# Kernel optimization log

Measured on AMD Instinct MI355X. Metric: run time of the kernel, lower is better.

The kernel has to match this reference:

```python
import jax, jax.numpy as jnp
import numpy as np

N, X_DIM, Z_DIM, H = 4096, 256, 128, 512
NUM_ACTIONS = 4
TEMPERATURE = 0.1


def _init_linear(key, fan_in, fan_out):
    kw, kb = jax.random.split(key)
    bound = 1.0 / np.sqrt(fan_in)
    W = jax.random.uniform(kw, (fan_in, fan_out), minval=-bound, maxval=bound, dtype=jnp.float32)
    b = jax.random.uniform(kb, (fan_out,), minval=-bound, maxval=bound, dtype=jnp.float32)
    return W, b


def setup_inputs() -> dict:
    key = jax.random.key(0)
    ks = jax.random.split(key, 9)
    s = jax.random.normal(ks[0], (N, X_DIM), dtype=jnp.float32)
    sp = jax.random.normal(ks[1], (N, X_DIM), dtype=jnp.float32)
    a = jax.random.randint(ks[2], (N,), 0, NUM_ACTIONS)
    a1h = jax.nn.one_hot(a, NUM_ACTIONS, dtype=jnp.float32)
    # phi: x_dim -> 512 -> 512 -> z_dim
    pW0, pb0 = _init_linear(ks[3], X_DIM, H)
    pW1, pb1 = _init_linear(ks[4], H, H)
    pW2, pb2 = _init_linear(ks[5], H, Z_DIM)
    # g: x_dim + 4 -> 512 -> 512 -> z_dim
    gW0, gb0 = _init_linear(ks[6], X_DIM + NUM_ACTIONS, H)
    gW1, gb1 = _init_linear(ks[7], H, H)
    gW2, gb2 = _init_linear(ks[8], H, Z_DIM)
    return {"s": s, "sp": sp, "a1h": a1h,
            "pW0": pW0, "pb0": pb0, "pW1": pW1, "pb1": pb1, "pW2": pW2, "pb2": pb2,
            "gW0": gW0, "gb0": gb0, "gW1": gW1, "gb1": gb1, "gW2": gW2, "gb2": gb2}


def _mlp(x, W0, b0, W1, b1, W2, b2):
    h = jax.nn.relu(x @ W0 + b0)
    h = jax.nn.relu(h @ W1 + b1)
    return h @ W2 + b2


def reference(s, sp, a1h, pW0, pb0, pW1, pb1, pW2, pb2, gW0, gb0, gW1, gb1, gW2, gb2):
    z = _mlp(s, pW0, pb0, pW1, pb1, pW2, pb2)                      # [N, D]
    zpos = _mlp(jnp.concatenate([sp, a1h], axis=-1), gW0, gb0, gW1, gb1, gW2, gb2)  # [N, D]
    # -||z_i - zpos_j||^2 / T via the GEMM trick (avoids the [N,N,D] diff tensor)
    sq_z = jnp.sum(z * z, axis=-1, keepdims=True)                  # [N, 1]
    sq_p = jnp.sum(zpos * zpos, axis=-1)                            # [N]
    logits = -(sq_z + sq_p[None, :] - 2.0 * z @ zpos.T) / TEMPERATURE  # [N, N]
    # cross-entropy with targets = arange(N): diagonal is the positive
    log_probs = jax.nn.log_softmax(logits, axis=-1)
    loss = -jnp.mean(jnp.diagonal(log_probs))
    return loss
```

## Files before the change

### kernel.cpp

```cpp
#include <hip/hip_runtime.h>
#include <math.h>

#define NR 4096
#define HD 512
#define NJR 32
#define INV_T 10.0f

typedef __attribute__((ext_vector_type(8))) short bf16x8;
typedef __attribute__((ext_vector_type(4))) short short4v;
typedef __attribute__((ext_vector_type(4))) float f32x4;

typedef const unsigned int __attribute__((address_space(1)))* gas_t;
typedef unsigned int __attribute__((address_space(3)))* las_t;

__device__ __forceinline__ unsigned short f2bf(float f) {
  union { float f; unsigned u; } v; v.f = f;
  unsigned r = v.u + 0x7fff + ((v.u >> 16) & 1);
  return (unsigned short)(r >> 16);
}
__device__ __forceinline__ float bf2f(unsigned short b) {
  union { unsigned u; float f; } v; v.u = ((unsigned)b) << 16;
  return v.f;
}


__global__ __launch_bounds__(256) void prep(
    const float* __restrict__ s, const float* __restrict__ sp,
    const float* __restrict__ a1h,
    unsigned short* __restrict__ Sb, unsigned short* __restrict__ SPb,
    int* __restrict__ aidx, float* __restrict__ sqp,
    const float* __restrict__ pW0, unsigned short* __restrict__ pW0t,
    const float* __restrict__ pW1, unsigned short* __restrict__ pW1t,
    const float* __restrict__ pW2, unsigned short* __restrict__ pW2t,
    const float* __restrict__ gW0, unsigned short* __restrict__ gW0t,
    const float* __restrict__ gW1, unsigned short* __restrict__ gW1t,
    const float* __restrict__ gW2, unsigned short* __restrict__ gW2t,
    float* __restrict__ out) {
  int b = blockIdx.x, tid = threadIdx.x;
  if (b < 16) {
    int r = b * 256 + tid;
    int a = 0;
#pragma unroll
    for (int j = 0; j < 4; ++j) if (a1h[(size_t)r * 4 + j] > 0.5f) a = j;
    aidx[r] = a;
    sqp[r] = 0.f;
    if (b == 0 && tid == 0) out[0] = 0.f;
    return;
  }
  const int idx8 = tid & 127;
  const int h = idx8 & 1, p = idx8 >> 1, hi = p >> 4, l15 = p & 15;
  if (b < 2064) {
    const float* src = (b < 1040) ? s : sp;
    unsigned short* dst = (b < 1040) ? Sb : SPb;
    int lb = (b < 1040) ? b - 16 : b - 1040;
    int s0 = lb * 2 + (tid >> 7);
    int rf = s0 >> 3, ks = s0 & 7;
    int row = rf * 16 + l15, c0 = ks * 32 + hi * 4 + h * 16;
    float4 v = *(const float4*)&src[(size_t)row * 256 + c0];
    short4v o = { (short)f2bf(v.x), (short)f2bf(v.y), (short)f2bf(v.z), (short)f2bf(v.w) };
    *(short4v*)((char*)dst + (size_t)s0 * 1024 + idx8 * 8) = o;
    return;
  }
  int local = b - 2064;
  const float* W; unsigned short* Wt; int N, ksh;
  if (local < 128)      { W = pW0; Wt = pW0t; N = 512; ksh = 3; }
  else if (local < 384) { W = pW1; Wt = pW1t; N = 512; ksh = 4; local -= 128; }
  else if (local < 448) { W = pW2; Wt = pW2t; N = 128; ksh = 4; local -= 384; }
  else if (local < 576) { W = gW0; Wt = gW0t; N = 512; ksh = 3; local -= 448; }
  else if (local < 832) { W = gW1; Wt = gW1t; N = 512; ksh = 4; local -= 576; }
  else                  { W = gW2; Wt = gW2t; N = 128; ksh = 4; local -= 832; }
  int s0 = local * 2 + (tid >> 7);
  int rf = s0 >> ksh, ks = s0 & ((1 << ksh) - 1);
  int n = rf * 16 + l15, k0 = ks * 32 + hi * 4 + h * 16;
  short4v o = { (short)f2bf(W[(size_t)(k0 + 0) * N + n]),
                (short)f2bf(W[(size_t)(k0 + 1) * N + n]),
                (short)f2bf(W[(size_t)(k0 + 2) * N + n]),
                (short)f2bf(W[(size_t)(k0 + 3) * N + n]) };
  *(short4v*)((char*)Wt + (size_t)s0 * 1024 + idx8 * 8) = o;
}

template <int BM, int BN, int K, bool RELU, bool GB, bool SQ>
__global__ __launch_bounds__(256) void gemm_db(
    const unsigned short* __restrict__ A0, const unsigned short* __restrict__ A1,
    const unsigned short* __restrict__ W0, const unsigned short* __restrict__ W1,
    const float* __restrict__ b0, const float* __restrict__ b1,
    unsigned short* __restrict__ C0, unsigned short* __restrict__ C1,
    float* __restrict__ sqp, int N,
    const int* __restrict__ aidx, const float* __restrict__ gW0f) {
  constexpr int KS = K >> 5;
  constexpr int NSTEP = K >> 6;
  constexpr int ABY = BM * 128;
  constexpr int BBY = BN * 128;
  constexpr int RFW = BM >> 5;
  constexpr int FNW = BN >> 5;
  constexpr int V = RFW + FNW;
  __shared__ char lds[2 * (ABY + BBY)];
  char* As = lds;
  char* Bs = lds + 2 * ABY;

  const int tid = threadIdx.x, lane = tid & 63, w = tid >> 6;
  const int wm = w >> 1, wn = w & 1;
  const int z = blockIdx.z;
  const char* Ab = (const char*)(z ? A1 : A0);
  const char* Wb = (const char*)(z ? W1 : W0);
  const float* bias = z ? b1 : b0;
  char* Cb = (char*)(z ? C1 : C0);
  const int bm = blockIdx.x * BM, bn = blockIdx.y * BN;
  const int lane16 = lane * 16;

  auto stage = [&](int buf, int st) {
#pragma unroll
    for (int u = 0; u < RFW; ++u) {
      const int sl = w * RFW + u;
      const char* src = Ab + ((size_t)((bm >> 4) + (sl >> 1)) * KS + st * 2 + (sl & 1)) * 1024 + lane16;
      __builtin_amdgcn_global_load_lds((gas_t)src, (las_t)(As + buf * ABY + sl * 1024), 16, 0, 0);
    }
#pragma unroll
    for (int u = 0; u < FNW; ++u) {
      const int sl = w * FNW + u;
      const char* src = Wb + ((size_t)((bn >> 4) + (sl >> 1)) * KS + st * 2 + (sl & 1)) * 1024 + lane16;
      __builtin_amdgcn_global_load_lds((gas_t)src, (las_t)(Bs + buf * BBY + sl * 1024), 16, 0, 0);
    }
  };

  f32x4 acc[RFW][FNW] = {};
  stage(0, 0);
#pragma unroll
  for (int st = 0; st < NSTEP; ++st) {
    const int buf = st & 1;
    if (st + 1 < NSTEP) {
      stage(buf ^ 1, st + 1);
      if constexpr (V == 4) asm volatile("s_waitcnt vmcnt(4)" ::: "memory");
      else                  asm volatile("s_waitcnt vmcnt(3)" ::: "memory");
    } else {
      asm volatile("s_waitcnt vmcnt(0)" ::: "memory");
    }
    __builtin_amdgcn_s_barrier();
#pragma unroll
    for (int kss = 0; kss < 2; ++kss) {
      bf16x8 af[RFW], bfv[FNW];
#pragma unroll
      for (int i = 0; i < RFW; ++i)
        af[i] = *(const bf16x8*)(As + buf * ABY + ((wm * RFW + i) * 2 + kss) * 1024 + lane16);
#pragma unroll
      for (int j = 0; j < FNW; ++j)
        bfv[j] = *(const bf16x8*)(Bs + buf * BBY + ((wn * FNW + j) * 2 + kss) * 1024 + lane16);
#pragma unroll
      for (int i = 0; i < RFW; ++i)
#pragma unroll
        for (int j = 0; j < FNW; ++j)
          acc[i][j] = __builtin_amdgcn_mfma_f32_16x16x32_bf16(bfv[j], af[i], acc[i][j], 0, 0, 0);
    }
    __builtin_amdgcn_s_barrier();
  }

  const int l15 = lane & 15, hi = lane >> 4;
  const int NS = N >> 5;
  const int row0 = bm + wm * (RFW * 16);
  const int col0 = bn + wn * (FNW * 16);
  int ar[RFW];
#pragma unroll
  for (int i = 0; i < RFW; ++i) ar[i] = 0;
  if (GB && z == 1) {
#pragma unroll
    for (int i = 0; i < RFW; ++i) ar[i] = aidx[row0 + i * 16 + l15];
  }
  if constexpr (FNW == 2) {
    float4 bi0 = *(const float4*)&bias[col0 + hi * 4];
    float4 bi1 = *(const float4*)&bias[col0 + 16 + hi * 4];
#pragma unroll
    for (int i = 0; i < RFW; ++i) {
      const int rfC = (row0 >> 4) + i;
      float v[8] = { acc[i][0][0] + bi0.x, acc[i][0][1] + bi0.y,
                     acc[i][0][2] + bi0.z, acc[i][0][3] + bi0.w,
                     acc[i][1][0] + bi1.x, acc[i][1][1] + bi1.y,
                     acc[i][1][2] + bi1.z, acc[i][1][3] + bi1.w };
      if (GB && z == 1) {
        float4 g0 = *(const float4*)&gW0f[(size_t)(256 + ar[i]) * N + col0 + hi * 4];
        float4 g1 = *(const float4*)&gW0f[(size_t)(256 + ar[i]) * N + col0 + 16 + hi * 4];
        v[0] += g0.x; v[1] += g0.y; v[2] += g0.z; v[3] += g0.w;
        v[4] += g1.x; v[5] += g1.y; v[6] += g1.z; v[7] += g1.w;
      }
      bf16x8 r;
#pragma unroll
      for (int t = 0; t < 8; ++t) {
        float vv = RELU ? fmaxf(v[t], 0.f) : v[t];
        r[t] = (short)f2bf(vv);
      }
      *(bf16x8*)(Cb + (size_t)(rfC * NS + (col0 >> 5)) * 1024 + lane16) = r;
    }
  } else {
    float4 bi0 = *(const float4*)&bias[col0 + hi * 4];
    float sq[RFW];
#pragma unroll
    for (int i = 0; i < RFW; ++i) sq[i] = 0.f;
#pragma unroll
    for (int i = 0; i < RFW; ++i) {
      const int rfC = (row0 >> 4) + i;
      float v[4] = { acc[i][0][0] + bi0.x, acc[i][0][1] + bi0.y,
                     acc[i][0][2] + bi0.z, acc[i][0][3] + bi0.w };
      short4v r;
#pragma unroll
      for (int t = 0; t < 4; ++t) {
        float vv = RELU ? fmaxf(v[t], 0.f) : v[t];
        unsigned short cv = f2bf(vv);
        r[t] = (short)cv;
        if (SQ) { float vb = bf2f(cv); sq[i] += vb * vb; }
      }
      *(short4v*)(Cb + (size_t)(rfC * NS + (bn >> 5)) * 1024 + lane16 + wn * 8) = r;
    }
    if (SQ && z == 1) {
#pragma unroll
      for (int i = 0; i < RFW; ++i) {
        float t = sq[i];
        t += __shfl_xor(t, 16, 64);
        t += __shfl_xor(t, 32, 64);
        if (lane < 16) atomicAdd(&sqp[row0 + i * 16 + lane], t);
      }
    }
  }
}

__global__ __launch_bounds__(256) void logits_fm(
    const unsigned short* __restrict__ Zb, const unsigned short* __restrict__ Zpb,
    const float* __restrict__ sqp, float* __restrict__ wm_,
    float* __restrict__ wsum, float* __restrict__ wdiag) {
  const int tid = threadIdx.x, lane = tid & 63, w = tid >> 6;
  const int l15 = lane & 15, hi = lane >> 4;
  const int i0 = blockIdx.x * 128, jr = blockIdx.y;
  const int row32 = i0 + w * 32;
  const int jbase = jr * 128;
  const int lane16 = lane * 16;
  const char* Zc = (const char*)Zb;
  const char* Pc = (const char*)Zpb;

  bf16x8 afr[2][4];
#pragma unroll
  for (int rf = 0; rf < 2; ++rf)
#pragma unroll
    for (int ks = 0; ks < 4; ++ks)
      afr[rf][ks] = *(const bf16x8*)(Zc + (size_t)(((row32 >> 4) + rf) * 4 + ks) * 1024 + lane16);

  f32x4 acc[2][8] = {};
#pragma unroll
  for (int jf = 0; jf < 8; ++jf) {
    const size_t js = (size_t)((jbase >> 4) + jf) * 4;
#pragma unroll
    for (int ks = 0; ks < 4; ++ks) {
      bf16x8 bfv = *(const bf16x8*)(Pc + (js + ks) * 1024 + lane16);
      acc[0][jf] = __builtin_amdgcn_mfma_f32_16x16x32_bf16(bfv, afr[0][ks], acc[0][jf], 0, 0, 0);
      acc[1][jf] = __builtin_amdgcn_mfma_f32_16x16x32_bf16(bfv, afr[1][ks], acc[1][jf], 0, 0, 0);
    }
  }

#pragma unroll
  for (int rf = 0; rf < 2; ++rf) {
    const int grow = row32 + rf * 16 + l15;
    float mx = -INFINITY, dd = 0.f;
    bool hasd = false;
#pragma unroll
    for (int jf = 0; jf < 8; ++jf) {
      const int cb = jbase + jf * 16 + hi * 4;
      float4 q = *(const float4*)&sqp[cb];
      float sp[4] = { q.x, q.y, q.z, q.w };
#pragma unroll
      for (int e = 0; e < 4; ++e) {
        float lv = (2.f * acc[rf][jf][e] - sp[e]) * INV_T;
        acc[rf][jf][e] = lv;
        mx = fmaxf(mx, lv);
        if (cb + e == grow) { dd = lv; hasd = true; }
      }
    }
    mx = fmaxf(mx, __shfl_xor(mx, 16, 64));
    mx = fmaxf(mx, __shfl_xor(mx, 32, 64));
    float sum = 0.f;
#pragma unroll
    for (int jf = 0; jf < 8; ++jf)
#pragma unroll
      for (int e = 0; e < 4; ++e) sum += __expf(acc[rf][jf][e] - mx);
    sum += __shfl_xor(sum, 16, 64);
    sum += __shfl_xor(sum, 32, 64);
    if (hi == 0) {
      wm_[(size_t)jr * NR + grow] = mx;
      wsum[(size_t)jr * NR + grow] = sum;
    }
    if (hasd) wdiag[grow] = dd;
  }
}

__global__ __launch_bounds__(256) void finalize(const float* __restrict__ wm,
    const float* __restrict__ wsum, const float* __restrict__ wdiag,
    float* __restrict__ out) {
  int r = blockIdx.x * 256 + threadIdx.x;
  float mm = wm[r];
  float ss = wsum[r];
#pragma unroll
  for (int p = 1; p < NJR; ++p) {
    float mo = wm[(size_t)p * NR + r];
    float so = wsum[(size_t)p * NR + r];
    float mn = fmaxf(mm, mo);
    ss = ss * __expf(mm - mn) + so * __expf(mo - mn);
    mm = mn;
  }
  float loss_r = mm + logf(ss) - wdiag[r];
  float v = loss_r;
#pragma unroll
  for (int off = 32; off; off >>= 1) v += __shfl_xor(v, off, 64);
  __shared__ float partial[4];
  if ((threadIdx.x & 63) == 0) partial[threadIdx.x >> 6] = v;
  __syncthreads();
  if (threadIdx.x == 0)
    atomicAdd(out, (partial[0] + partial[1] + partial[2] + partial[3]) * (1.0f / (float)NR));
}

extern "C" void kernel_launch(void* const* d_in, const int* in_sizes, int n_in,
                              void* d_out, int out_size, void* d_ws, size_t ws_size,
                              hipStream_t stream) {
  const float* s   = (const float*)d_in[0];
  const float* sp  = (const float*)d_in[1];
  const float* a1h = (const float*)d_in[2];
  const float* pW0 = (const float*)d_in[3];
  const float* pb0 = (const float*)d_in[4];
  const float* pW1 = (const float*)d_in[5];
  const float* pb1 = (const float*)d_in[6];
  const float* pW2 = (const float*)d_in[7];
  const float* pb2 = (const float*)d_in[8];
  const float* gW0 = (const float*)d_in[9];
  const float* gb0 = (const float*)d_in[10];
  const float* gW1 = (const float*)d_in[11];
  const float* gb1 = (const float*)d_in[12];
  const float* gW2 = (const float*)d_in[13];
  const float* gb2 = (const float*)d_in[14];

  char* p = (char*)d_ws;
  unsigned short* Sb   = (unsigned short*)p; p += (size_t)NR * 256 * 2;
  unsigned short* SPb  = (unsigned short*)p; p += (size_t)NR * 256 * 2;
  unsigned short* H1   = (unsigned short*)p; p += (size_t)2 * NR * HD * 2;
  unsigned short* H2   = (unsigned short*)p; p += (size_t)2 * NR * HD * 2;
  unsigned short* Zall = (unsigned short*)p; p += (size_t)2 * NR * 128 * 2;
  unsigned short* pW0t = (unsigned short*)p; p += (size_t)256 * 512 * 2;
  unsigned short* pW1t = (unsigned short*)p; p += (size_t)512 * 512 * 2;
  unsigned short* pW2t = (unsigned short*)p; p += (size_t)512 * 128 * 2;
  unsigned short* gW0t = (unsigned short*)p; p += (size_t)256 * 512 * 2;
  unsigned short* gW1t = (unsigned short*)p; p += (size_t)512 * 512 * 2;
  unsigned short* gW2t = (unsigned short*)p; p += (size_t)512 * 128 * 2;
  float* sqp  = (float*)p; p += (size_t)NR * 4;
  float* wm   = (float*)p; p += (size_t)NJR * NR * 4;
  float* wsm  = (float*)p; p += (size_t)NJR * NR * 4;
  float* wdg  = (float*)p; p += (size_t)NR * 4;
  int*   aidx = (int*)p;  p += (size_t)NR * 4;

  unsigned short* H1g = H1 + (size_t)NR * HD;
  unsigned short* H2g = H2 + (size_t)NR * HD;
  unsigned short* Zb  = Zall;
  unsigned short* Zpb = Zall + (size_t)NR * 128;

  dim3 blk(256);
  prep<<<2960, blk, 0, stream>>>(s, sp, a1h, Sb, SPb, aidx, sqp,
                                 pW0, pW0t, pW1, pW1t, pW2, pW2t,
                                 gW0, gW0t, gW1, gW1t, gW2, gW2t,
                                 (float*)d_out);

  gemm_db<64, 64, 256, true, true, false><<<dim3(64, 8, 2), blk, 0, stream>>>(
      Sb, SPb, pW0t, gW0t, pb0, gb0, H1, H1g, nullptr, 512, aidx, gW0);
  gemm_db<64, 64, 512, true, false, false><<<dim3(64, 8, 2), blk, 0, stream>>>(
      H1, H1g, pW1t, gW1t, pb1, gb1, H2, H2g, nullptr, 512, nullptr, nullptr);
  gemm_db<64, 32, 512, false, false, true><<<dim3(64, 4, 2), blk, 0, stream>>>(
      H2, H2g, pW2t, gW2t, pb2, gb2, Zb, Zpb, sqp, 128, nullptr, nullptr);

  logits_fm<<<dim3(NR / 128, NJR), blk, 0, stream>>>(Zb, Zpb, sqp, wm, wsm, wdg);
  finalize<<<NR / 256, blk, 0, stream>>>(wm, wsm, wdg, (float*)d_out);
}
```

Baseline: 57.32 us.

## Fuse input conversion into layer-0 GEMM and finalize into logits kernel

The first layer now reads fp32 inputs and weights directly, converting to bf16 in registers and writing the tiled LDS layout itself. This removes the separate bf16 copies of s/sp and the W0 transposes, and folds the action-index decode into the epilogue. The squared-norm atomics become per-column-block partial sums, and the logits kernel now stages Zpos tiles in LDS. The last blocks of the logits kernel, chosen through an atomic counter with a spin-wait, run the final log-sum-exp reduction, which removes two launches. The trade-off is an uncoalesced scalar-scatter B write in layer 0 and a spin-wait that depends on all blocks being scheduled.

Result: slower. 69.25 us (+20.8%).

```diff
diff --git a/kernel.cpp b/kernel.cpp
--- a/kernel.cpp
+++ b/kernel.cpp
@@ -5,6 +5,7 @@
 #define HD 512
 #define NJR 32
 #define INV_T 10.0f
+#define DONE_FINAL 1024
 
 typedef __attribute__((ext_vector_type(8))) short bf16x8;
 typedef __attribute__((ext_vector_type(4))) short short4v;
@@ -24,80 +25,166 @@
 }
 
 
-__global__ __launch_bounds__(256) void prep(
+__global__ __launch_bounds__(256) void l0_fused(
     const float* __restrict__ s, const float* __restrict__ sp,
     const float* __restrict__ a1h,
-    unsigned short* __restrict__ Sb, unsigned short* __restrict__ SPb,
-    int* __restrict__ aidx, float* __restrict__ sqp,
-    const float* __restrict__ pW0, unsigned short* __restrict__ pW0t,
+    const float* __restrict__ pW0, const float* __restrict__ gW0,
+    const float* __restrict__ pb0, const float* __restrict__ gb0,
+    unsigned short* __restrict__ H1p, unsigned short* __restrict__ H1g,
     const float* __restrict__ pW1, unsigned short* __restrict__ pW1t,
     const float* __restrict__ pW2, unsigned short* __restrict__ pW2t,
-    const float* __restrict__ gW0, unsigned short* __restrict__ gW0t,
     const float* __restrict__ gW1, unsigned short* __restrict__ gW1t,
-    const float* __restrict__ gW2, unsigned short* __restrict__ gW2t,
-    float* __restrict__ out) {
-  int b = blockIdx.x, tid = threadIdx.x;
-  if (b < 16) {
-    int r = b * 256 + tid;
-    int a = 0;
-#pragma unroll
-    for (int j = 0; j < 4; ++j) if (a1h[(size_t)r * 4 + j] > 0.5f) a = j;
-    aidx[r] = a;
-    sqp[r] = 0.f;
-    if (b == 0 && tid == 0) out[0] = 0.f;
+    const float* __restrict__ gW2, unsigned short* __restrict__ gW2t) {
+  const int bid = blockIdx.x, tid = threadIdx.x;
+  if (bid >= 1024) {
+    int local = bid - 1024;
+    const float* W; unsigned short* Wt; int N;
+    if (local < 256)      { W = pW1; Wt = pW1t; N = 512; }
+    else if (local < 320) { W = pW2; Wt = pW2t; N = 128; local -= 256; }
+    else if (local < 576) { W = gW1; Wt = gW1t; N = 512; local -= 320; }
+    else                  { W = gW2; Wt = gW2t; N = 128; local -= 576; }
+    const int idx8 = tid & 127;
+    const int h = idx8 & 1, p = idx8 >> 1, hi = p >> 4, l15 = p & 15;
+    int s0 = local * 2 + (tid >> 7);
+    int rf = s0 >> 4, ks = s0 & 15;
+    int n = rf * 16 + l15, k0 = ks * 32 + hi * 4 + h * 16;
+    short4v o = { (short)f2bf(W[(size_t)(k0 + 0) * N + n]),
+                  (short)f2bf(W[(size_t)(k0 + 1) * N + n]),
+                  (short)f2bf(W[(size_t)(k0 + 2) * N + n]),
+                  (short)f2bf(W[(size_t)(k0 + 3) * N + n]) };
+    *(short4v*)((char*)Wt + (size_t)s0 * 1024 + idx8 * 8) = o;
     return;
   }
-  const int idx8 = tid & 127;
-  const int h = idx8 & 1, p = idx8 >> 1, hi = p >> 4, l15 = p & 15;
-  if (b < 2064) {
-    const float* src = (b < 1040) ? s : sp;
-    unsigned short* dst = (b < 1040) ? Sb : SPb;
-    int lb = (b < 1040) ? b - 16 : b - 1040;
-    int s0 = lb * 2 + (tid >> 7);
-    int rf = s0 >> 3, ks = s0 & 7;
-    int row = rf * 16 + l15, c0 = ks * 32 + hi * 4 + h * 16;
-    float4 v = *(const float4*)&src[(size_t)row * 256 + c0];
-    short4v o = { (short)f2bf(v.x), (short)f2bf(v.y), (short)f2bf(v.z), (short)f2bf(v.w) };
-    *(short4v*)((char*)dst + (size_t)s0 * 1024 + idx8 * 8) = o;
-    return;
-  }
-  int local = b - 2064;
-  const float* W; unsigned short* Wt; int N, ksh;
-  if (local < 128)      { W = pW0; Wt = pW0t; N = 512; ksh = 3; }
-  else if (local < 384) { W = pW1; Wt = pW1t; N = 512; ksh = 4; local -= 128; }
-  else if (local < 448) { W = pW2; Wt = pW2t; N = 128; ksh = 4; local -= 384; }
-  else if (local < 576) { W = gW0; Wt = gW0t; N = 512; ksh = 3; local -= 448; }
-  else if (local < 832) { W = gW1; Wt = gW1t; N = 512; ksh = 4; local -= 576; }
-  else                  { W = gW2; Wt = gW2t; N = 128; ksh = 4; local -= 832; }
-  int s0 = local * 2 + (tid >> 7);
-  int rf = s0 >> ksh, ks = s0 & ((1 << ksh) - 1);
-  int n = rf * 16 + l15, k0 = ks * 32 + hi * 4 + h * 16;
-  short4v o = { (short)f2bf(W[(size_t)(k0 + 0) * N + n]),
-                (short)f2bf(W[(size_t)(k0 + 1) * N + n]),
-                (short)f2bf(W[(size_t)(k0 + 2) * N + n]),
-                (short)f2bf(W[(size_t)(k0 + 3) * N + n]) };
-  *(short4v*)((char*)Wt + (size_t)s0 * 1024 + idx8 * 8) = o;
-}
-
-template <int BM, int BN, int K, bool RELU, bool GB, bool SQ>
-__global__ __launch_bounds__(256) void gemm_db(
+  __shared__ __align__(1024) char As[2][8192];
+  __shared__ __align__(1024) char Bs[2][8192];
+  const int z = bid >> 9, rem = bid & 511;
+  const int bx = rem & 63, by = rem >> 6;
+  const float* A = z ? sp : s;
+  const float* W = z ? gW0 : pW0;
+  const float* bias = z ? gb0 : pb0;
+  unsigned short* C = z ? H1g : H1p;
+  const int lane = tid & 63, w = tid >> 6;
+  const int wm = w >> 1, wn = w & 1;
+  const int bm = bx * 64, bn = by * 64;
+  const int lane16 = lane * 16;
+
+  int aslot[2], ale[2], arow[2], akb[2];
+#pragma unroll
+  for (int q = 0; q < 2; ++q) {
+    int e = q * 256 + tid;
+    aslot[q] = e >> 6; ale[q] = e & 63;
+    arow[q] = bm + (aslot[q] >> 1) * 16 + (ale[q] & 15);
+    akb[q] = (aslot[q] & 1) * 32 + (ale[q] >> 4) * 4;
+  }
+  int bk[4], bn4[4];
+#pragma unroll
+  for (int r = 0; r < 4; ++r) {
+    int idx = r * 256 + tid;
+    bk[r] = idx >> 4; bn4[r] = (idx & 15) * 4;
+  }
+  float4 fa[2][2], fb[4];
+  auto loadAB = [&](int k0) {
+#pragma unroll
+    for (int q = 0; q < 2; ++q) {
+      fa[q][0] = *(const float4*)&A[(size_t)arow[q] * 256 + k0 + akb[q]];
+      fa[q][1] = *(const float4*)&A[(size_t)arow[q] * 256 + k0 + akb[q] + 16];
+    }
+#pragma unroll
+    for (int r = 0; r < 4; ++r)
+      fb[r] = *(const float4*)&W[(size_t)(k0 + bk[r]) * 512 + bn + bn4[r]];
+  };
+  auto writeAB = [&](int buf) {
+#pragma unroll
+    for (int q = 0; q < 2; ++q) {
+      bf16x8 o;
+      o[0] = (short)f2bf(fa[q][0].x); o[1] = (short)f2bf(fa[q][0].y);
+      o[2] = (short)f2bf(fa[q][0].z); o[3] = (short)f2bf(fa[q][0].w);
+      o[4] = (short)f2bf(fa[q][1].x); o[5] = (short)f2bf(fa[q][1].y);
+      o[6] = (short)f2bf(fa[q][1].z); o[7] = (short)f2bf(fa[q][1].w);
+      *(bf16x8*)(As[buf] + aslot[q] * 1024 + ale[q] * 16) = o;
+    }
+#pragma unroll
+    for (int r = 0; r < 4; ++r) {
+      const int k_l = bk[r], ks = k_l >> 5, w32 = k_l & 31;
+      const int hi = (w32 & 15) >> 2, d = w32 & 3, h = (w32 >> 4) & 1;
+      const float* fp = reinterpret_cast<const float*>(&fb[r]);
+#pragma unroll
+      for (int j = 0; j < 4; ++j) {
+        const int n = bn4[r] + j;
+        *(unsigned short*)(Bs[buf] + ((n >> 4) * 2 + ks) * 1024 +
+                           ((hi * 16 + (n & 15)) * 16) + h * 8 + d * 2) = f2bf(fp[j]);
+      }
+    }
+  };
+
+  f32x4 acc[2][2] = {};
+  loadAB(0);
+#pragma unroll
+  for (int st = 0; st < 4; ++st) {
+    const int buf = st & 1;
+    writeAB(buf);
+    __syncthreads();
+    if (st < 3) loadAB((st + 1) * 64);
+#pragma unroll
+    for (int kss = 0; kss < 2; ++kss) {
+      bf16x8 af[2], bfv[2];
+#pragma unroll
+      for (int i = 0; i < 2; ++i)
+        af[i] = *(const bf16x8*)(As[buf] + ((wm * 2 + i) * 2 + kss) * 1024 + lane16);
+#pragma unroll
+      for (int j = 0; j < 2; ++j)
+        bfv[j] = *(const bf16x8*)(Bs[buf] + ((wn * 2 + j) * 2 + kss) * 1024 + lane16);
+#pragma unroll
+      for (int i = 0; i < 2; ++i)
+#pragma unroll
+        for (int j = 0; j < 2; ++j)
+          acc[i][j] = __builtin_amdgcn_mfma_f32_16x16x32_bf16(bfv[j], af[i], acc[i][j], 0, 0, 0);
+    }
+    __syncthreads();
+  }
+
+  const int l15 = lane & 15, hi = lane >> 4;
+  const int row0 = bm + wm * 32;
+  const int col0 = bn + wn * 32;
+  int ar[2] = {0, 0};
+  if (z == 1) {
+#pragma unroll
+    for (int i = 0; i < 2; ++i) {
+      float4 aa = *(const float4*)&a1h[(size_t)(row0 + i * 16 + l15) * 4];
+      ar[i] = (aa.y > 0.5f) ? 1 : (aa.z > 0.5f) ? 2 : (aa.w > 0.5f) ? 3 : 0;
+    }
+  }
+  float4 bi0 = *(const float4*)&bias[col0 + hi * 4];
+  float4 bi1 = *(const float4*)&bias[col0 + 16 + hi * 4];
+#pragma unroll
+  for (int i = 0; i < 2; ++i) {
+    const int rfC = (row0 >> 4) + i;
+    float v[8] = { acc[i][0][0] + bi0.x, acc[i][0][1] + bi0.y,
+                   acc[i][0][2] + bi0.z, acc[i][0][3] + bi0.w,
+                   acc[i][1][0] + bi1.x, acc[i][1][1] + bi1.y,
+                   acc[i][1][2] + bi1.z, acc[i][1][3] + bi1.w };
+    if (z == 1) {
+      float4 g0 = *(const float4*)&gW0[(size_t)(256 + ar[i]) * 512 + col0 + hi * 4];
+      float4 g1 = *(const float4*)&gW0[(size_t)(256 + ar[i]) * 512 + col0 + 16 + hi * 4];
+      v[0] += g0.x; v[1] += g0.y; v[2] += g0.z; v[3] += g0.w;
+      v[4] += g1.x; v[5] += g1.y; v[6] += g1.z; v[7] += g1.w;
+    }
+    bf16x8 r;
+#pragma unroll
+    for (int t = 0; t < 8; ++t) r[t] = (short)f2bf(fmaxf(v[t], 0.f));
+    *(bf16x8*)((char*)C + (size_t)(rfC * 16 + (col0 >> 5)) * 1024 + lane16) = r;
+  }
+}
+
+__global__ __launch_bounds__(256) void gemm_mid(
     const unsigned short* __restrict__ A0, const unsigned short* __restrict__ A1,
     const unsigned short* __restrict__ W0, const unsigned short* __restrict__ W1,
     const float* __restrict__ b0, const float* __restrict__ b1,
-    unsigned short* __restrict__ C0, unsigned short* __restrict__ C1,
-    float* __restrict__ sqp, int N,
-    const int* __restrict__ aidx, const float* __restrict__ gW0f) {
-  constexpr int KS = K >> 5;
-  constexpr int NSTEP = K >> 6;
-  constexpr int ABY = BM * 128;
-  constexpr int BBY = BN * 128;
-  constexpr int RFW = BM >> 5;
-  constexpr int FNW = BN >> 5;
-  constexpr int V = RFW + FNW;
-  __shared__ char lds[2 * (ABY + BBY)];
+    unsigned short* __restrict__ C0, unsigned short* __restrict__ C1) {
+  constexpr int K = 512, KS = K >> 5, NSTEP = K >> 6, N = 512;
+  __shared__ char lds[2 * 16384];
   char* As = lds;
-  char* Bs = lds + 2 * ABY;
-
+  char* Bs = lds + 16384;
   const int tid = threadIdx.x, lane = tid & 63, w = tid >> 6;
   const int wm = w >> 1, wn = w & 1;
   const int z = blockIdx.z;
@@ -105,153 +192,205 @@
   const char* Wb = (const char*)(z ? W1 : W0);
   const float* bias = z ? b1 : b0;
   char* Cb = (char*)(z ? C1 : C0);
-  const int bm = blockIdx.x * BM, bn = blockIdx.y * BN;
+  const int bm = blockIdx.x * 64, bn = blockIdx.y * 64;
   const int lane16 = lane * 16;
 
   auto stage = [&](int buf, int st) {
 #pragma unroll
-    for (int u = 0; u < RFW; ++u) {
-      const int sl = w * RFW + u;
-      const char* src = Ab + ((size_t)((bm >> 4) + (sl >> 1)) * KS + st * 2 + (sl & 1)) * 1024 + lane16;
-      __builtin_amdgcn_global_load_lds((gas_t)src, (las_t)(As + buf * ABY + sl * 1024), 16, 0, 0);
-    }
-#pragma unroll
-    for (int u = 0; u < FNW; ++u) {
-      const int sl = w * FNW + u;
-      const char* src = Wb + ((size_t)((bn >> 4) + (sl >> 1)) * KS + st * 2 + (sl & 1)) * 1024 + lane16;
-      __builtin_amdgcn_global_load_lds((gas_t)src, (las_t)(Bs + buf * BBY + sl * 1024), 16, 0, 0);
+    for (int u = 0; u < 2; ++u) {
+      const int sl = w * 2 + u;
+      const char* srcA = Ab + ((size_t)((bm >> 4) + (sl >> 1)) * KS + st * 2 + (sl & 1)) * 1024 + lane16;
+      __builtin_amdgcn_global_load_lds((gas_t)srcA, (las_t)(As + buf * 8192 + sl * 1024), 16, 0, 0);
+      const char* srcB = Wb + ((size_t)((bn >> 4) + (sl >> 1)) * KS + st * 2 + (sl & 1)) * 1024 + lane16;
+      __builtin_amdgcn_global_load_lds((gas_t)srcB, (las_t)(Bs + buf * 8192 + sl * 1024), 16, 0, 0);
     }
   };
 
-  f32x4 acc[RFW][FNW] = {};
+  f32x4 acc[2][2] = {};
   stage(0, 0);
 #pragma unroll
   for (int st = 0; st < NSTEP; ++st) {
     const int buf = st & 1;
     if (st + 1 < NSTEP) {
       stage(buf ^ 1, st + 1);
-      if constexpr (V == 4) asm volatile("s_waitcnt vmcnt(4)" ::: "memory");
-      else                  asm volatile("s_waitcnt vmcnt(3)" ::: "memory");
+      asm volatile("s_waitcnt vmcnt(4)" ::: "memory");
     } else {
       asm volatile("s_waitcnt vmcnt(0)" ::: "memory");
     }
     __builtin_amdgcn_s_barrier();
 #pragma unroll
     for (int kss = 0; kss < 2; ++kss) {
-      bf16x8 af[RFW], bfv[FNW];
-#pragma unroll
-      for (int i = 0; i < RFW; ++i)
-        af[i] = *(const bf16x8*)(As + buf * ABY + ((wm * RFW + i) * 2 + kss) * 1024 + lane16);
-#pragma unroll
-      for (int j = 0; j < FNW; ++j)
-        bfv[j] = *(const bf16x8*)(Bs + buf * BBY + ((wn * FNW + j) * 2 + kss) * 1024 + lane16);
-#pragma unroll
-      for (int i = 0; i < RFW; ++i)
-#pragma unroll
-        for (int j = 0; j < FNW; ++j)
+      bf16x8 af[2], bfv[2];
+#pragma unroll
+      for (int i = 0; i < 2; ++i)
+        af[i] = *(const bf16x8*)(As + buf * 8192 + ((wm * 2 + i) * 2 + kss) * 1024 + lane16);
+#pragma unroll
+      for (int j = 0; j < 2; ++j)
+        bfv[j] = *(const bf16x8*)(Bs + buf * 8192 + ((wn * 2 + j) * 2 + kss) * 1024 + lane16);
+#pragma unroll
+      for (int i = 0; i < 2; ++i)
+#pragma unroll
+        for (int j = 0; j < 2; ++j)
           acc[i][j] = __builtin_amdgcn_mfma_f32_16x16x32_bf16(bfv[j], af[i], acc[i][j], 0, 0, 0);
     }
     __builtin_amdgcn_s_barrier();
   }
 
   const int l15 = lane & 15, hi = lane >> 4;
-  const int NS = N >> 5;
-  const int row0 = bm + wm * (RFW * 16);
-  const int col0 = bn + wn * (FNW * 16);
-  int ar[RFW];
-#pragma unroll
-  for (int i = 0; i < RFW; ++i) ar[i] = 0;
-  if (GB && z == 1) {
-#pragma unroll
-    for (int i = 0; i < RFW; ++i) ar[i] = aidx[row0 + i * 16 + l15];
-  }
-  if constexpr (FNW == 2) {
-    float4 bi0 = *(const float4*)&bias[col0 + hi * 4];
-    float4 bi1 = *(const float4*)&bias[col0 + 16 + hi * 4];
-#pragma unroll
-    for (int i = 0; i < RFW; ++i) {
-      const int rfC = (row0 >> 4) + i;
-      float v[8] = { acc[i][0][0] + bi0.x, acc[i][0][1] + bi0.y,
-                     acc[i][0][2] + bi0.z, acc[i][0][3] + bi0.w,
-                     acc[i][1][0] + bi1.x, acc[i][1][1] + bi1.y,
-                     acc[i][1][2] + bi1.z, acc[i][1][3] + bi1.w };
-      if (GB && z == 1) {
-        float4 g0 = *(const float4*)&gW0f[(size_t)(256 + ar[i]) * N + col0 + hi * 4];
-        float4 g1 = *(const float4*)&gW0f[(size_t)(256 + ar[i]) * N + col0 + 16 + hi * 4];
-        v[0] += g0.x; v[1] += g0.y; v[2] += g0.z; v[3] += g0.w;
-        v[4] += g1.x; v[5] += g1.y; v[6] += g1.z; v[7] += g1.w;
-      }
-      bf16x8 r;
-#pragma unroll
-      for (int t = 0; t < 8; ++t) {
-        float vv = RELU ? fmaxf(v[t], 0.f) : v[t];
-        r[t] = (short)f2bf(vv);
-      }
-      *(bf16x8*)(Cb + (size_t)(rfC * NS + (col0 >> 5)) * 1024 + lane16) = r;
-    }
-  } else {
-    float4 bi0 = *(const float4*)&bias[col0 + hi * 4];
-    float sq[RFW];
-#pragma unroll
-    for (int i = 0; i < RFW; ++i) sq[i] = 0.f;
-#pragma unroll
-    for (int i = 0; i < RFW; ++i) {
-      const int rfC = (row0 >> 4) + i;
-      float v[4] = { acc[i][0][0] + bi0.x, acc[i][0][1] + bi0.y,
-                     acc[i][0][2] + bi0.z, acc[i][0][3] + bi0.w };
-      short4v r;
-#pragma unroll
-      for (int t = 0; t < 4; ++t) {
-        float vv = RELU ? fmaxf(v[t], 0.f) : v[t];
-        unsigned short cv = f2bf(vv);
-        r[t] = (short)cv;
-        if (SQ) { float vb = bf2f(cv); sq[i] += vb * vb; }
-      }
-      *(short4v*)(Cb + (size_t)(rfC * NS + (bn >> 5)) * 1024 + lane16 + wn * 8) = r;
-    }
-    if (SQ && z == 1) {
-#pragma unroll
-      for (int i = 0; i < RFW; ++i) {
-        float t = sq[i];
-        t += __shfl_xor(t, 16, 64);
-        t += __shfl_xor(t, 32, 64);
-        if (lane < 16) atomicAdd(&sqp[row0 + i * 16 + lane], t);
-      }
-    }
-  }
-}
-
-__global__ __launch_bounds__(256) void logits_fm(
+  const int row0 = bm + wm * 32, col0 = bn + wn * 32;
+  float4 bi0 = *(const float4*)&bias[col0 + hi * 4];
+  float4 bi1 = *(const float4*)&bias[col0 + 16 + hi * 4];
+#pragma unroll
+  for (int i = 0; i < 2; ++i) {
+    const int rfC = (row0 >> 4) + i;
+    float v[8] = { acc[i][0][0] + bi0.x, acc[i][0][1] + bi0.y,
+                   acc[i][0][2] + bi0.z, acc[i][0][3] + bi0.w,
+                   acc[i][1][0] + bi1.x, acc[i][1][1] + bi1.y,
+                   acc[i][1][2] + bi1.z, acc[i][1][3] + bi1.w };
+    bf16x8 r;
+#pragma unroll
+    for (int t = 0; t < 8; ++t) r[t] = (short)f2bf(fmaxf(v[t], 0.f));
+    *(bf16x8*)(Cb + (size_t)(rfC * (N >> 5) + (col0 >> 5)) * 1024 + lane16) = r;
+  }
+}
+
+__global__ __launch_bounds__(256) void gemm_l2(
+    const unsigned short* __restrict__ A0, const unsigned short* __restrict__ A1,
+    const unsigned short* __restrict__ W0, const unsigned short* __restrict__ W1,
+    const float* __restrict__ b0, const float* __restrict__ b1,
+    unsigned short* __restrict__ C0, unsigned short* __restrict__ C1,
+    float* __restrict__ sqp4, unsigned* __restrict__ done, float* __restrict__ out) {
+  constexpr int K = 512, KS = K >> 5, NSTEP = K >> 6, N = 128;
+  __shared__ char lds[2 * 12288];
+  char* As = lds;
+  char* Bs = lds + 16384;
+  __shared__ float sqred[2][64];
+  const int tid = threadIdx.x, lane = tid & 63, w = tid >> 6;
+  const int wm = w >> 1, wn = w & 1;
+  const int z = blockIdx.z;
+  if (blockIdx.x == 0 && blockIdx.y == 0 && z == 0) {
+    for (int i = tid; i < 1025; i += 256) done[i] = 0;
+    if (tid == 0) out[0] = 0.f;
+  }
+  const char* Ab = (const char*)(z ? A1 : A0);
+  const char* Wb = (const char*)(z ? W1 : W0);
+  const float* bias = z ? b1 : b0;
+  char* Cb = (char*)(z ? C1 : C0);
+  const int bm = blockIdx.x * 64, bn = blockIdx.y * 32;
+  const int lane16 = lane * 16;
+
+  auto stage = [&](int buf, int st) {
+#pragma unroll
+    for (int u = 0; u < 2; ++u) {
+      const int sl = w * 2 + u;
+      const char* srcA = Ab + ((size_t)((bm >> 4) + (sl >> 1)) * KS + st * 2 + (sl & 1)) * 1024 + lane16;
+      __builtin_amdgcn_global_load_lds((gas_t)srcA, (las_t)(As + buf * 8192 + sl * 1024), 16, 0, 0);
+    }
+    const int sl = w;
+    const char* srcB = Wb + ((size_t)((bn >> 4) + (sl >> 1)) * KS + st * 2 + (sl & 1)) * 1024 + lane16;
+    __builtin_amdgcn_global_load_lds((gas_t)srcB, (las_t)(Bs + buf * 4096 + sl * 1024), 16, 0, 0);
+  };
+
+  f32x4 acc[2] = {};
+  stage(0, 0);
+#pragma unroll
+  for (int st = 0; st < NSTEP; ++st) {
+    const int buf = st & 1;
+    if (st + 1 < NSTEP) {
+      stage(buf ^ 1, st + 1);
+      asm volatile("s_waitcnt vmcnt(3)" ::: "memory");
+    } else {
+      asm volatile("s_waitcnt vmcnt(0)" ::: "memory");
+    }
+    __builtin_amdgcn_s_barrier();
+#pragma unroll
+    for (int kss = 0; kss < 2; ++kss) {
+      bf16x8 af[2], bfv;
+#pragma unroll
+      for (int i = 0; i < 2; ++i)
+        af[i] = *(const bf16x8*)(As + buf * 8192 + ((wm * 2 + i) * 2 + kss) * 1024 + lane16);
+      bfv = *(const bf16x8*)(Bs + buf * 4096 + (wn * 2 + kss) * 1024 + lane16);
+#pragma unroll
+      for (int i = 0; i < 2; ++i)
+        acc[i] = __builtin_amdgcn_mfma_f32_16x16x32_bf16(bfv, af[i], acc[i], 0, 0, 0);
+    }
+    __builtin_amdgcn_s_barrier();
+  }
+
+  const int l15 = lane & 15, hi = lane >> 4;
+  const int row0 = bm + wm * 32;
+  const int col0 = bn + wn * 16;
+  float4 bi0 = *(const float4*)&bias[col0 + hi * 4];
+  float sq[2] = {0.f, 0.f};
+#pragma unroll
+  for (int i = 0; i < 2; ++i) {
+    const int rfC = (row0 >> 4) + i;
+    float v[4] = { acc[i][0] + bi0.x, acc[i][1] + bi0.y, acc[i][2] + bi0.z, acc[i][3] + bi0.w };
+    short4v r;
+#pragma unroll
+    for (int t = 0; t < 4; ++t) {
+      unsigned short cv = f2bf(v[t]);
+      r[t] = (short)cv;
+      float vb = bf2f(cv);
+      sq[i] += vb * vb;
+    }
+    *(short4v*)(Cb + (size_t)(rfC * (N >> 5) + (bn >> 5)) * 1024 + lane16 + wn * 8) = r;
+  }
+#pragma unroll
+  for (int i = 0; i < 2; ++i) {
+    float t = sq[i];
+    t += __shfl_xor(t, 16, 64);
+    t += __shfl_xor(t, 32, 64);
+    if (lane < 16) sqred[wn][wm * 32 + i * 16 + lane] = t;
+  }
+  __syncthreads();
+  if (z == 1 && tid < 64)
+    sqp4[(size_t)blockIdx.y * NR + bm + tid] = sqred[0][tid] + sqred[1][tid];
+}
+
+__global__ __launch_bounds__(256) void logits_fin(
     const unsigned short* __restrict__ Zb, const unsigned short* __restrict__ Zpb,
-    const float* __restrict__ sqp, float* __restrict__ wm_,
-    float* __restrict__ wsum, float* __restrict__ wdiag) {
+    const float* __restrict__ sqp4, float* __restrict__ wm_,
+    float* __restrict__ wsum, float* __restrict__ wdiag,
+    unsigned* __restrict__ done, float* __restrict__ out) {
+  __shared__ __align__(1024) char Ps[32768];
+  __shared__ int hid;
+  __shared__ float fpart[4];
   const int tid = threadIdx.x, lane = tid & 63, w = tid >> 6;
   const int l15 = lane & 15, hi = lane >> 4;
-  const int i0 = blockIdx.x * 128, jr = blockIdx.y;
+  const int bx = blockIdx.x, jr = blockIdx.y;
+  const int i0 = bx * 128;
   const int row32 = i0 + w * 32;
   const int jbase = jr * 128;
   const int lane16 = lane * 16;
   const char* Zc = (const char*)Zb;
   const char* Pc = (const char*)Zpb;
 
+#pragma unroll
+  for (int u = 0; u < 8; ++u) {
+    const int sl = w * 8 + u;
+    __builtin_amdgcn_global_load_lds(
+        (gas_t)(Pc + ((size_t)(jbase >> 4) * 4 + sl) * 1024 + lane16),
+        (las_t)(Ps + sl * 1024), 16, 0, 0);
+  }
   bf16x8 afr[2][4];
 #pragma unroll
   for (int rf = 0; rf < 2; ++rf)
 #pragma unroll
     for (int ks = 0; ks < 4; ++ks)
       afr[rf][ks] = *(const bf16x8*)(Zc + (size_t)(((row32 >> 4) + rf) * 4 + ks) * 1024 + lane16);
+  asm volatile("s_waitcnt vmcnt(0)" ::: "memory");
+  __syncthreads();
 
   f32x4 acc[2][8] = {};
 #pragma unroll
-  for (int jf = 0; jf < 8; ++jf) {
-    const size_t js = (size_t)((jbase >> 4) + jf) * 4;
-#pragma unroll
-    for (int ks = 0; ks < 4; ++ks) {
-      bf16x8 bfv = *(const bf16x8*)(Pc + (js + ks) * 1024 + lane16);
+  for (int ks = 0; ks < 4; ++ks)
+#pragma unroll
+    for (int jf = 0; jf < 8; ++jf) {
+      bf16x8 bfv = *(const bf16x8*)(Ps + (jf * 4 + ks) * 1024 + lane16);
       acc[0][jf] = __builtin_amdgcn_mfma_f32_16x16x32_bf16(bfv, afr[0][ks], acc[0][jf], 0, 0, 0);
       acc[1][jf] = __builtin_amdgcn_mfma_f32_16x16x32_bf16(bfv, afr[1][ks], acc[1][jf], 0, 0, 0);
     }
-  }
 
 #pragma unroll
   for (int rf = 0; rf < 2; ++rf) {
@@ -261,8 +400,12 @@
 #pragma unroll
     for (int jf = 0; jf < 8; ++jf) {
       const int cb = jbase + jf * 16 + hi * 4;
-      float4 q = *(const float4*)&sqp[cb];
-      float sp[4] = { q.x, q.y, q.z, q.w };
+      float4 q0 = *(const float4*)&sqp4[cb];
+      float4 q1 = *(const float4*)&sqp4[NR + cb];
+      float4 q2 = *(const float4*)&sqp4[2 * NR + cb];
+      float4 q3 = *(const float4*)&sqp4[3 * NR + cb];
+      float sp[4] = { q0.x + q1.x + q2.x + q3.x, q0.y + q1.y + q2.y + q3.y,
+                      q0.z + q1.z + q2.z + q3.z, q0.w + q1.w + q2.w + q3.w };
 #pragma unroll
       for (int e = 0; e < 4; ++e) {
         float lv = (2.f * acc[rf][jf][e] - sp[e]) * INV_T;
@@ -286,31 +429,47 @@
     }
     if (hasd) wdiag[grow] = dd;
   }
-}
-
-__global__ __launch_bounds__(256) void finalize(const float* __restrict__ wm,
-    const float* __restrict__ wsum, const float* __restrict__ wdiag,
-    float* __restrict__ out) {
-  int r = blockIdx.x * 256 + threadIdx.x;
-  float mm = wm[r];
-  float ss = wsum[r];
-#pragma unroll
-  for (int p = 1; p < NJR; ++p) {
-    float mo = wm[(size_t)p * NR + r];
-    float so = wsum[(size_t)p * NR + r];
-    float mn = fmaxf(mm, mo);
-    ss = ss * __expf(mm - mn) + so * __expf(mo - mn);
-    mm = mn;
-  }
-  float loss_r = mm + logf(ss) - wdiag[r];
-  float v = loss_r;
-#pragma unroll
-  for (int off = 32; off; off >>= 1) v += __shfl_xor(v, off, 64);
-  __shared__ float partial[4];
-  if ((threadIdx.x & 63) == 0) partial[threadIdx.x >> 6] = v;
+
   __syncthreads();
-  if (threadIdx.x == 0)
-    atomicAdd(out, (partial[0] + partial[1] + partial[2] + partial[3]) * (1.0f / (float)NR));
+  if (tid == 0) {
+    hid = -1;
+    const int bid = jr * 32 + bx;
+    unsigned old = __hip_atomic_fetch_add(&done[(bid & 63) * 16], 1u,
+                                          __ATOMIC_RELEASE, __HIP_MEMORY_SCOPE_AGENT);
+    if (old == 15u) {
+      unsigned f = __hip_atomic_fetch_add(&done[DONE_FINAL], 1u,
+                                          __ATOMIC_RELEASE, __HIP_MEMORY_SCOPE_AGENT);
+      if (f >= 48u) {
+        while (__hip_atomic_load(&done[DONE_FINAL], __ATOMIC_ACQUIRE,
+                                 __HIP_MEMORY_SCOPE_AGENT) < 64u)
+          __builtin_amdgcn_s_sleep(16);
+        hid = (int)(f - 48u);
+      }
+    }
+  }
+  __syncthreads();
+  if (hid < 0) return;
+
+  {
+    const int r = hid * 256 + tid;
+    float mm = wm_[r];
+    float ss = wsum[r];
+#pragma unroll
+    for (int p = 1; p < NJR; ++p) {
+      float mo = wm_[(size_t)p * NR + r];
+      float so = wsum[(size_t)p * NR + r];
+      float mn = fmaxf(mm, mo);
+      ss = ss * __expf(mm - mn) + so * __expf(mo - mn);
+      mm = mn;
+    }
+    float v = mm + logf(ss) - wdiag[r];
+#pragma unroll
+    for (int off = 32; off; off >>= 1) v += __shfl_xor(v, off, 64);
+    if (lane == 0) fpart[w] = v;
+    __syncthreads();
+    if (tid == 0)
+      atomicAdd(out, (fpart[0] + fpart[1] + fpart[2] + fpart[3]) * (1.0f / (float)NR));
+  }
 }
 
 extern "C" void kernel_launch(void* const* d_in, const int* in_sizes, int n_in,
@@ -333,22 +492,18 @@
   const float* gb2 = (const float*)d_in[14];
 
   char* p = (char*)d_ws;
-  unsigned short* Sb   = (unsigned short*)p; p += (size_t)NR * 256 * 2;
-  unsigned short* SPb  = (unsigned short*)p; p += (size_t)NR * 256 * 2;
   unsigned short* H1   = (unsigned short*)p; p += (size_t)2 * NR * HD * 2;
   unsigned short* H2   = (unsigned short*)p; p += (size_t)2 * NR * HD * 2;
   unsigned short* Zall = (unsigned short*)p; p += (size_t)2 * NR * 128 * 2;
-  unsigned short* pW0t = (unsigned short*)p; p += (size_t)256 * 512 * 2;
   unsigned short* pW1t = (unsigned short*)p; p += (size_t)512 * 512 * 2;
   unsigned short* pW2t = (unsigned short*)p; p += (size_t)512 * 128 * 2;
-  unsigned short* gW0t = (unsigned short*)p; p += (size_t)256 * 512 * 2;
   unsigned short* gW1t = (unsigned short*)p; p += (size_t)512 * 512 * 2;
   unsigned short* gW2t = (unsigned short*)p; p += (size_t)512 * 128 * 2;
-  float* sqp  = (float*)p; p += (size_t)NR * 4;
+  float* sqp4 = (float*)p; p += (size_t)4 * NR * 4;
   float* wm   = (float*)p; p += (size_t)NJR * NR * 4;
   float* wsm  = (float*)p; p += (size_t)NJR * NR * 4;
   float* wdg  = (float*)p; p += (size_t)NR * 4;
-  int*   aidx = (int*)p;  p += (size_t)NR * 4;
+  unsigned* done = (unsigned*)p; p += 8192;
 
   unsigned short* H1g = H1 + (size_t)NR * HD;
   unsigned short* H2g = H2 + (size_t)NR * HD;
@@ -356,18 +511,11 @@
   unsigned short* Zpb = Zall + (size_t)NR * 128;
 
   dim3 blk(256);
-  prep<<<2960, blk, 0, stream>>>(s, sp, a1h, Sb, SPb, aidx, sqp,
-                                 pW0, pW0t, pW1, pW1t, pW2, pW2t,
-                                 gW0, gW0t, gW1, gW1t, gW2, gW2t,
-                                 (float*)d_out);
-
-  gemm_db<64, 64, 256, true, true, false><<<dim3(64, 8, 2), blk, 0, stream>>>(
-      Sb, SPb, pW0t, gW0t, pb0, gb0, H1, H1g, nullptr, 512, aidx, gW0);
-  gemm_db<64, 64, 512, true, false, false><<<dim3(64, 8, 2), blk, 0, stream>>>(
-      H1, H1g, pW1t, gW1t, pb1, gb1, H2, H2g, nullptr, 512, nullptr, nullptr);
-  gemm_db<64, 32, 512, false, false, true><<<dim3(64, 4, 2), blk, 0, stream>>>(
-      H2, H2g, pW2t, gW2t, pb2, gb2, Zb, Zpb, sqp, 128, nullptr, nullptr);
-
-  logits_fm<<<dim3(NR / 128, NJR), blk, 0, stream>>>(Zb, Zpb, sqp, wm, wsm, wdg);
-  finalize<<<NR / 256, blk, 0, stream>>>(wm, wsm, wdg, (float*)d_out);
-}
+  l0_fused<<<1664, blk, 0, stream>>>(s, sp, a1h, pW0, gW0, pb0, gb0, H1, H1g,
+                                     pW1, pW1t, pW2, pW2t, gW1, gW1t, gW2, gW2t);
+  gemm_mid<<<dim3(64, 8, 2), blk, 0, stream>>>(H1, H1g, pW1t, gW1t, pb1, gb1, H2, H2g);
+  gemm_l2<<<dim3(64, 4, 2), blk, 0, stream>>>(H2, H2g, pW2t, gW2t, pb2, gb2, Zb, Zpb,
+                                              sqp4, done, (float*)d_out);
+  logits_fin<<<dim3(32, 32), blk, 0, stream>>>(Zb, Zpb, sqp4, wm, wsm, wdg,
+                                               done, (float*)d_out);
+}
```
